# Kernel tuning notes

Hardware: AMD Instinct MI355X
Metric: run time of the kernel (lower is better)

Reference implementation:

```python
import math
import jax, jax.numpy as jnp
import numpy as np

B, H, M, L, D, HID = 4, 8, 1024, 3200, 128, 1024
ATTN_LIM, RAMP = 2048, 128
PRE_DIV, LOSS_COEF = 16.0, 1e-06
SIZE = ATTN_LIM  # ExpireSpanDrop size = args.attn_lim


def skew(X, pad_value):
    # X: (BH, M, K) -> (BH, M, K+M), shifting row i right by i (relative-pos trick)
    BH, Mq, K = X.shape
    X = jnp.pad(X, ((0, 0), (0, 0), (0, Mq + 1)), constant_values=pad_value)
    X = X.reshape(BH, -1)[:, :-Mq]
    return X.reshape(BH, Mq, K + Mq)


def setup_inputs():
    key = jax.random.key(0)
    ks = jax.random.split(key, 6)
    query = jax.random.normal(ks[0], (B * H, M, D), jnp.float32)
    k = jax.random.normal(ks[1], (B * H, L, D), jnp.float32)
    v = jax.random.normal(ks[2], (B * H, L, D), jnp.float32)
    memory_hid = jax.random.normal(ks[3], (B, L, HID), jnp.float32)
    # age counters: oldest slot first; the current block (last M slots) goes down to -(M-1)
    memory_counter = jnp.broadcast_to(
        jnp.arange(L - 1, -1, -1, dtype=jnp.float32) - (M - 1), (B, L))
    key_pe = 0.02 * jax.random.normal(ks[4], (1, D, M), jnp.float32)
    span_w = 0.01 * jax.random.normal(ks[5], (1, HID), jnp.float32)
    span_b = jnp.full((1,), -math.log(1.0 / 0.1 - 1.0), jnp.float32)  # init_percentage=0.1
    return {"query": query, "key": k, "value": v, "memory_hid": memory_hid,
            "memory_counter": memory_counter, "key_pe": key_pe,
            "span_w": span_w, "span_b": span_b}


def reference(query, key, value, memory_hid, memory_counter, key_pe, span_w, span_b):
    max_mem = ATTN_LIM + M + RAMP
    # QK^T
    attn = jnp.einsum('bmd,bld->bml', query, key)                              # (BH, M, L)
    # --- ExpireSpanDrop (eval mode, no noise) ---
    max_span = jax.nn.sigmoid(
        jnp.einsum('blh,oh->blo', memory_hid / PRE_DIV, span_w)[..., 0] + span_b[0]) * SIZE  # (B, L)
    remaining_offset = max_span - memory_counter                               # (B, L)
    remaining_span = remaining_offset[:, None, :] - jnp.arange(M, dtype=jnp.float32)[None, :, None]  # (B, M, L)
    emask = jnp.clip(remaining_span / RAMP + 1.0, 0.0, 1.0)
    ramp_mask = ((emask > 0) & (emask < 1)).astype(emask.dtype)
    aux_loss = (remaining_span * ramp_mask).sum((-1, -2)) / RAMP / M * LOSS_COEF  # (B,)
    # causal mask (precomputed buffer in torch)
    causal = jnp.tril(jnp.ones((M, max_mem), jnp.float32), k=max_mem - M - 1)[:, -L:]
    mask = jnp.broadcast_to((emask * causal)[:, None], (B, H, M, L)).reshape(B * H, M, L)
    # --- relative position bias via skew ---
    attn_pos = skew(jnp.einsum('bmd,dk->bmk', query, key_pe[0]), 0.0)          # (BH, M, 2M)
    attn = attn.at[:, :, -2 * M:].add(attn_pos)
    # masked softmax + renormalization by soft mask
    attn = jnp.where(mask == 0, -jnp.inf, attn) / math.sqrt(D)
    attn = jax.nn.softmax(attn, axis=-1)
    attn = attn * mask
    attn = attn / (attn.sum(-1, keepdims=True) + 1e-08)
    out = jnp.einsum('bml,bld->bmd', attn, value)                              # (BH, M, D)
    return out, aux_loss, remaining_offset
```

## Files before the change

### kernel.cpp

```cpp
#include <hip/hip_runtime.h>
#include <stdint.h>

#define B_   4
#define H_   8
#define BH_  32
#define M_   1024
#define L_   3200
#define D_   128
#define HID_ 1024
#define NT64 50
#define CAUSAL_K 2175
#define POS_OFF  1152
#define SCALE 0.08838834764831845f
#define NEGV (-3.0e38f)
#define NEGH (-1.0e38f)

typedef short  bf16x8 __attribute__((ext_vector_type(8)));
typedef float  f32x4  __attribute__((ext_vector_type(4)));

__device__ __forceinline__ unsigned short f2bf(float x) {
    union { float f; uint32_t u; } v; v.f = x;
    return (unsigned short)((v.u + 0x7FFFu + ((v.u >> 16) & 1u)) >> 16);
}
__device__ __forceinline__ float bf2f(unsigned short h) {
    union { uint32_t u; float f; } v; v.u = ((uint32_t)h) << 16; return v.f;
}
__device__ __forceinline__ uint32_t pack_bf2(float lo, float hi) {
    union { float f; uint32_t u; } a, b; a.f = lo; b.f = hi;
    return __builtin_amdgcn_perm(b.u, a.u, 0x07060302u);
}

template <int CTRL>
__device__ __forceinline__ float dpp_movf(float x) {
    union { float f; int i; } u; u.f = x;
    u.i = __builtin_amdgcn_update_dpp(0, u.i, CTRL, 0xF, 0xF, true);
    return u.f;
}
__device__ __forceinline__ float row_max16(float x) {
    x = fmaxf(x, dpp_movf<0xB1>(x));
    x = fmaxf(x, dpp_movf<0x4E>(x));
    x = fmaxf(x, dpp_movf<0x141>(x));
    x = fmaxf(x, dpp_movf<0x140>(x));
    return x;
}
__device__ __forceinline__ float row_sum16(float x) {
    x += dpp_movf<0xB1>(x);
    x += dpp_movf<0x4E>(x);
    x += dpp_movf<0x141>(x);
    x += dpp_movf<0x140>(x);
    return x;
}

__global__ void span_kernel(const float* __restrict__ hid,
                            const float* __restrict__ counter,
                            const float* __restrict__ sw,
                            const float* __restrict__ sb,
                            float* __restrict__ r0_ws,
                            float* __restrict__ r0_out) {
    const int row  = blockIdx.x * 4 + (threadIdx.x >> 6);
    const int lane = threadIdx.x & 63;
    const float* h = hid + (size_t)row * HID_;
    float acc = 0.f;
#pragma unroll
    for (int it = 0; it < 4; ++it) {
        const int k = it * 256 + lane * 4;
        const float4 a = *(const float4*)(h + k);
        const float4 w = *(const float4*)(sw + k);
        acc += a.x*w.x + a.y*w.y + a.z*w.z + a.w*w.w;
    }
#pragma unroll
    for (int off = 32; off; off >>= 1) acc += __shfl_down(acc, off);
    if (lane == 0) {
        const float x  = acc * (1.0f/16.0f) + sb[0];
        const float ms = 2048.0f / (1.0f + __expf(-x));
        const float r0 = ms - counter[row];
        r0_ws[row]  = r0;
        r0_out[row] = r0;
    }
}

__global__ void tilemax_kernel(const float* __restrict__ r0_ws,
                               float* __restrict__ tmax) {
    const int t = blockIdx.x;
    const int lane = threadIdx.x;
    float v = r0_ws[t * 64 + lane];
#pragma unroll
    for (int off = 32; off; off >>= 1) v = fmaxf(v, __shfl_down(v, off));
    if (lane == 0) tmax[t] = v;
}

__global__ void aux_kernel(const float* __restrict__ r0_ws,
                           float* __restrict__ aux_out) {
    const int b = blockIdx.x, tid = threadIdx.x;
    float s = 0.f;
    for (int l = tid; l < L_; l += 256) {
        const float r = r0_ws[b * L_ + l];
        const int fl = (int)floorf(r);
        int mlo = fl + 1;   if (mlo < 0) mlo = 0;
        int mhi = fl + 128; if (mhi > M_ - 1) mhi = M_ - 1;
        const int n = mhi - mlo + 1;
        if (n > 0) s += (float)n * r - 0.5f * (float)(mlo + mhi) * (float)n;
    }
    __shared__ float red[256];
    red[tid] = s; __syncthreads();
    for (int st = 128; st; st >>= 1) {
        if (tid < st) red[tid] += red[tid + st];
        __syncthreads();
    }
    if (tid == 0) aux_out[b] = red[0] * (1.0f/128.0f) * (1.0f/1024.0f) * 1e-6f;
}

__global__ void pet_kernel(const float* __restrict__ PE,
                           unsigned short* __restrict__ PET) {
    const int tid = threadIdx.x;
    const int c = blockIdx.x * 4 + (tid >> 6);
    const int e = tid & 63;
    const float lo = PE[(2*e)   * M_ + c];
    const float hi = PE[(2*e+1) * M_ + c];
    ((uint32_t*)PET)[c * 64 + e] = pack_bf2(lo, hi);
}

#define KS_STR 136
#define VT_STR 72
#define PE_STR 136
#define P_STR  72
#define T_STR  72

__global__ void __launch_bounds__(256, 2)
attn_kernel(const float* __restrict__ Q, const float* __restrict__ K,
            const float* __restrict__ V, const unsigned short* __restrict__ PET,
            const float* __restrict__ r0g, const float* __restrict__ tmax,
            float* __restrict__ out) {
    __shared__ short Ks[64 * KS_STR];
    __shared__ short Vt[128 * VT_STR];
    __shared__ short PEs[64 * PE_STR];
    __shared__ short Tb[2][64 * T_STR];
    __shared__ short Pb[64 * P_STR];
    __shared__ float r0s[64];
    __shared__ float tfl[NT64];

    const int bh = blockIdx.y;
    const int b  = bh >> 3;
    const int i0 = blockIdx.x << 6;
    const int tid  = threadIdx.x;
    const int wave = tid >> 6;
    const int lane = tid & 63;
    const int lq   = lane & 15;
    const int quad = lane >> 4;
    const int lt_end = min(NT64, (int)blockIdx.x + 35);

    if (tid < NT64) tfl[tid] = tmax[b * NT64 + tid];
    __syncthreads();
    const float live_thresh = (float)(i0 - 128);

    auto next_live = [&](int s) {
        while (s < lt_end && !(tfl[s] > live_thresh)) ++s;
        return s;
    };

    float4 kp[8];
    float4 vpa[4], vpb[4];
    uint4  pep[4];
    float  r0p = 0.f;

    auto issue_prefetch = [&](int plt) {
        const int l0p = plt << 6;
        const float* kb = K + ((size_t)bh * L_ + l0p) * D_;
        const float* vb = V + ((size_t)bh * L_ + l0p) * D_;
#pragma unroll
        for (int it = 0; it < 8; ++it) {
            const int f = it * 256 + tid;
            kp[it] = *(const float4*)(kb + (f >> 5) * D_ + (f & 31) * 4);
        }
        const int p2 = (tid & 31) * 2;
#pragma unroll
        for (int it = 0; it < 4; ++it) {
            const int c = it * 8 + (tid >> 5);
            vpa[it] = *(const float4*)(vb + (size_t)p2 * D_ + c * 4);
            vpb[it] = *(const float4*)(vb + (size_t)(p2 + 1) * D_ + c * 4);
        }
        const int c0p = l0p - i0 - POS_OFF;
#pragma unroll
        for (int it = 0; it < 4; ++it) {
            const int f = it * 256 + tid;
            const int cg = c0p + (f >> 4);
            if ((unsigned)cg < (unsigned)M_)
                pep[it] = *(const uint4*)(PET + (size_t)cg * D_ + (f & 15) * 8);
            else { pep[it].x = 0; pep[it].y = 0; pep[it].z = 0; pep[it].w = 0; }
        }
        if (tid < 64) r0p = r0g[b * L_ + l0p + tid];
    };

    auto write_stage = [&]() {
#pragma unroll
        for (int it = 0; it < 8; ++it) {
            const int f = it * 256 + tid;
            uint2 w;
            w.x = pack_bf2(kp[it].x, kp[it].y);
            w.y = pack_bf2(kp[it].z, kp[it].w);
            *(uint2*)&Ks[(f >> 5) * KS_STR + (f & 31) * 4] = w;
        }
        const int p2 = (tid & 31) * 2;
#pragma unroll
        for (int it = 0; it < 4; ++it) {
            const int c = it * 8 + (tid >> 5);
            const float* a = (const float*)&vpa[it];
            const float* bb = (const float*)&vpb[it];
#pragma unroll
            for (int j = 0; j < 4; ++j)
                *(uint32_t*)&Vt[(c * 4 + j) * VT_STR + p2] = pack_bf2(a[j], bb[j]);
        }
#pragma unroll
        for (int it = 0; it < 4; ++it) {
            const int f = it * 256 + tid;
            *(uint4*)&PEs[(f >> 4) * PE_STR + (f & 15) * 8] = pep[it];
        }
        if (tid < 64) r0s[tid] = r0p;
    };

    int lt = next_live(0);
    if (lt < lt_end) issue_prefetch(lt);

    bf16x8 qfrag[4];
    {
        const float* qp = Q + ((size_t)bh * M_ + (i0 + wave * 16 + lq)) * D_;
#pragma unroll
        for (int kk = 0; kk < 4; ++kk) {
            const float4 q0 = *(const float4*)(qp + kk * 32 + quad * 8);
            const float4 q1 = *(const float4*)(qp + kk * 32 + quad * 8 + 4);
            union { bf16x8 v; uint32_t u[4]; } qq;
            qq.u[0] = pack_bf2(q0.x, q0.y); qq.u[1] = pack_bf2(q0.z, q0.w);
            qq.u[2] = pack_bf2(q1.x, q1.y); qq.u[3] = pack_bf2(q1.z, q1.w);
            qfrag[kk] = qq.v;
        }
    }

    auto computeT = [&](short* tb) {
#pragma unroll
        for (int nt = 0; nt < 4; ++nt) {
            f32x4 acc = (f32x4){0.f, 0.f, 0.f, 0.f};
#pragma unroll
            for (int kk = 0; kk < 4; ++kk) {
                const bf16x8 bf = *(const bf16x8*)&PEs[(nt*16 + lq) * PE_STR + kk*32 + quad*8];
                acc = __builtin_amdgcn_mfma_f32_16x16x32_bf16(qfrag[kk], bf, acc, 0, 0, 0);
            }
#pragma unroll
            for (int r = 0; r < 4; ++r) {
                union { float f; uint32_t u; } t; t.f = acc[r];
                tb[(wave*16 + quad*4 + r) * T_STR + nt*16 + lq] = (short)(t.u >> 16);
            }
        }
    };

    f32x4 oacc[8];
#pragma unroll
    for (int d = 0; d < 8; ++d) oacc[d] = (f32x4){0.f, 0.f, 0.f, 0.f};
    float mrun[4] = {NEGV, NEGV, NEGV, NEGV};
    float Zr[4]   = {0.f, 0.f, 0.f, 0.f};
    float Zm[4]   = {0.f, 0.f, 0.f, 0.f};
    int tlo = 0, thi = 1;
    int prev_c0 = -(1 << 30);

    while (lt < lt_end) {
        const int l0 = lt << 6;
        const int c0 = l0 - i0 - POS_OFF;
        const bool need_pos = (c0 + 63 >= 0) && (c0 - 63 <= M_ - 1);
        const bool rolling  = need_pos && (prev_c0 == c0 - 64);

        __syncthreads();
        write_stage();
        __syncthreads();

        const int ltn = next_live(lt + 1);
        if (ltn < lt_end) issue_prefetch(ltn);

        f32x4 sfrag[4];
#pragma unroll
        for (int nt = 0; nt < 4; ++nt) {
            f32x4 acc = (f32x4){0.f, 0.f, 0.f, 0.f};
#pragma unroll
            for (int kk = 0; kk < 4; ++kk) {
                const bf16x8 bf = *(const bf16x8*)&Ks[(nt*16 + lq) * KS_STR + kk*32 + quad*8];
                acc = __builtin_amdgcn_mfma_f32_16x16x32_bf16(qfrag[kk], bf, acc, 0, 0, 0);
            }
            sfrag[nt] = acc;
        }

        if (need_pos) {
            if (rolling) {
                const int t = tlo; tlo = thi; thi = t;
                computeT(&Tb[thi][0]);
            } else {
                tlo = 0; thi = 1;
                computeT(&Tb[1][0]);
                uint4 lowp[4];
#pragma unroll
                for (int it = 0; it < 4; ++it) {
                    const int f = it * 256 + tid;
                    const int cg = (c0 - 64) + (f >> 4);
                    if ((unsigned)cg < (unsigned)M_)
                        lowp[it] = *(const uint4*)(PET + (size_t)cg * D_ + (f & 15) * 8);
                    else { lowp[it].x = 0; lowp[it].y = 0; lowp[it].z = 0; lowp[it].w = 0; }
                }
                __syncthreads();
#pragma unroll
                for (int it = 0; it < 4; ++it) {
                    const int f = it * 256 + tid;
                    *(uint4*)&PEs[(f >> 4) * PE_STR + (f & 15) * 8] = lowp[it];
                }
                __syncthreads();
                computeT(&Tb[0][0]);
            }
            prev_c0 = c0;
        } else {
            prev_c0 = -(1 << 30);
        }

        float rv[4];
#pragma unroll
        for (int nt = 0; nt < 4; ++nt) rv[nt] = r0s[nt*16 + lq];

        float sv[4][4], em[4][4];
#pragma unroll
        for (int r = 0; r < 4; ++r) {
            const int iq = i0 + wave*16 + quad*4 + r;
            const float fiq = (float)iq;
#pragma unroll
            for (int nt = 0; nt < 4; ++nt) {
                const int l = l0 + nt*16 + lq;
                float s = sfrag[nt][r];
                const int c = l - iq - POS_OFF;
                if (need_pos && (unsigned)c < (unsigned)M_) {
                    const int cb = c - (c0 - 64);
                    const short* tbp = (cb & 64) ? &Tb[thi][0] : &Tb[tlo][0];
                    s += bf2f((unsigned short)tbp[(wave*16 + quad*4 + r) * T_STR + (cb & 63)]);
                }
                const float e = fminf(fmaxf((rv[nt] - fiq) * 0.0078125f + 1.0f, 0.f), 1.f);
                em[r][nt] = e;
                const bool live = (l <= iq + CAUSAL_K) && (e > 0.f);
                sv[r][nt] = live ? s * SCALE : NEGV;
            }
        }

#pragma unroll
        for (int r = 0; r < 4; ++r) {
            float v = fmaxf(fmaxf(sv[r][0], sv[r][1]), fmaxf(sv[r][2], sv[r][3]));
            v = row_max16(v);
            const float nm = fmaxf(mrun[r], v);
            float alpha = 1.f, psum = 0.f, pmsum = 0.f, pmv[4];
            if (nm > NEGH) {
                alpha = (mrun[r] > NEGH) ? __expf(mrun[r] - nm) : 0.f;
#pragma unroll
                for (int nt = 0; nt < 4; ++nt) {
                    const float p = __expf(sv[r][nt] - nm);
                    const float pm = p * em[r][nt];
                    psum += p; pmsum += pm; pmv[nt] = pm;
                }
            } else {
                pmv[0] = pmv[1] = pmv[2] = pmv[3] = 0.f;
            }
            psum  = row_sum16(psum);
            pmsum = row_sum16(pmsum);
            mrun[r] = nm;
            Zr[r] = Zr[r] * alpha + psum;
            Zm[r] = Zm[r] * alpha + pmsum;
#pragma unroll
            for (int d = 0; d < 8; ++d) oacc[d][r] *= alpha;
#pragma unroll
            for (int nt = 0; nt < 4; ++nt) {
                union { float f; uint32_t u; } t; t.f = pmv[nt];
                Pb[(wave*16 + quad*4 + r) * P_STR + nt*16 + lq] = (short)(t.u >> 16);
            }
        }

#pragma unroll
        for (int kk = 0; kk < 2; ++kk) {
            const bf16x8 pf = *(const bf16x8*)&Pb[(wave*16 + lq) * P_STR + kk*32 + quad*8];
#pragma unroll
            for (int dt = 0; dt < 8; ++dt) {
                const bf16x8 vf = *(const bf16x8*)&Vt[(dt*16 + lq) * VT_STR + kk*32 + quad*8];
                oacc[dt] = __builtin_amdgcn_mfma_f32_16x16x32_bf16(pf, vf, oacc[dt], 0, 0, 0);
            }
        }
        lt = ltn;
    }

#pragma unroll
    for (int r = 0; r < 4; ++r) {
        const int iq = i0 + wave*16 + quad*4 + r;
        const float inv = 1.0f / (Zm[r] + 1e-8f * Zr[r]);
        float* op = out + ((size_t)bh * M_ + iq) * D_;
#pragma unroll
        for (int dt = 0; dt < 8; ++dt)
            op[dt*16 + lq] = oacc[dt][r] * inv;
    }
}

__global__ void __launch_bounds__(256, 2)
attn_fb_kernel(const float* __restrict__ Q, const float* __restrict__ K,
               const float* __restrict__ V, const float* __restrict__ PE,
               const float* __restrict__ r0g, const float* __restrict__ tmax,
               float* __restrict__ out) {
    __shared__ short Ks[64 * KS_STR];
    __shared__ short Vt[128 * VT_STR];
    __shared__ short PEP[64 * PE_STR];
    __shared__ short Tb[2][64 * T_STR];
    __shared__ float r0s[64];

    const int bh = blockIdx.y;
    const int b  = bh >> 3;
    const int i0 = blockIdx.x << 6;
    const int tid  = threadIdx.x;
    const int wave = tid >> 6;
    const int lane = tid & 63;
    const int lq   = lane & 15;
    const int quad = lane >> 4;

    bf16x8 qfrag[4];
    {
        const float* qp = Q + ((size_t)bh * M_ + (i0 + wave * 16 + lq)) * D_;
#pragma unroll
        for (int kk = 0; kk < 4; ++kk) {
            const float* p = qp + kk * 32 + quad * 8;
            bf16x8 f;
#pragma unroll
            for (int j = 0; j < 8; ++j) f[j] = (short)f2bf(p[j]);
            qfrag[kk] = f;
        }
    }

    f32x4 oacc[8];
#pragma unroll
    for (int d = 0; d < 8; ++d) oacc[d] = (f32x4){0.f, 0.f, 0.f, 0.f};
    float mrun[4] = {NEGV, NEGV, NEGV, NEGV};
    float Zr[4]   = {0.f, 0.f, 0.f, 0.f};
    float Zm[4]   = {0.f, 0.f, 0.f, 0.f};

    int tlo = 0, thi = 1;
    int prev_c0 = -100000;

    auto stagePE = [&](int cbase) {
#pragma unroll
        for (int it = 0; it < 8; ++it) {
            const int f4 = it * 256 + tid;
            const int d  = f4 >> 4;
            const int cl = (f4 & 15) << 2;
#pragma unroll
            for (int j = 0; j < 4; ++j) {
                const int cg = cbase + cl + j;
                const float v = (cg >= 0 && cg < M_) ? PE[d * M_ + cg] : 0.f;
                PEP[(cl + j) * PE_STR + d] = (short)f2bf(v);
            }
        }
    };
    auto computeT = [&](short* tb) {
#pragma unroll
        for (int nt = 0; nt < 4; ++nt) {
            f32x4 acc = (f32x4){0.f, 0.f, 0.f, 0.f};
#pragma unroll
            for (int kk = 0; kk < 4; ++kk) {
                const bf16x8 bf = *(const bf16x8*)&PEP[(nt*16 + lq) * PE_STR + kk*32 + quad*8];
                acc = __builtin_amdgcn_mfma_f32_16x16x32_bf16(qfrag[kk], bf, acc, 0, 0, 0);
            }
#pragma unroll
            for (int r = 0; r < 4; ++r)
                tb[(wave*16 + quad*4 + r) * T_STR + nt*16 + lq] = (short)f2bf(acc[r]);
        }
    };

    const int lt_end = min(NT64, (int)blockIdx.x + 35);
    for (int lt = 0; lt < lt_end; ++lt) {
        const int l0 = lt << 6;
        if (!(tmax[b * NT64 + lt] > (float)(i0 - 128))) continue;

        __syncthreads();
        {
            const float* kbase = K + ((size_t)bh * L_ + l0) * D_;
            const float* vbase = V + ((size_t)bh * L_ + l0) * D_;
#pragma unroll
            for (int it = 0; it < 8; ++it) {
                const int f4 = it * 256 + tid;
                const int row = f4 >> 5;
                const int ds  = (f4 & 31) << 2;
                const float4 kv = *(const float4*)(kbase + row * D_ + ds);
                uint2 pk;
                pk.x = (uint32_t)f2bf(kv.x) | ((uint32_t)f2bf(kv.y) << 16);
                pk.y = (uint32_t)f2bf(kv.z) | ((uint32_t)f2bf(kv.w) << 16);
                *(uint2*)&Ks[row * KS_STR + ds] = pk;
                const float4 vv = *(const float4*)(vbase + row * D_ + ds);
                Vt[(ds+0) * VT_STR + row] = (short)f2bf(vv.x);
                Vt[(ds+1) * VT_STR + row] = (short)f2bf(vv.y);
                Vt[(ds+2) * VT_STR + row] = (short)f2bf(vv.z);
                Vt[(ds+3) * VT_STR + row] = (short)f2bf(vv.w);
            }
            if (tid < 64) r0s[tid] = r0g[b * L_ + l0 + tid];
        }

        const int c0 = l0 - i0 - POS_OFF;
        const bool need_pos = (c0 + 63 >= 0) && (c0 - 63 <= M_ - 1);
        if (need_pos) {
            if (prev_c0 == c0 - 64) {
                const int t = tlo; tlo = thi; thi = t;
                stagePE(c0);
                __syncthreads();
                computeT(&Tb[thi][0]);
            } else {
                stagePE(c0 - 64);
                __syncthreads();
                computeT(&Tb[0][0]);
                __syncthreads();
                stagePE(c0);
                __syncthreads();
                computeT(&Tb[1][0]);
                tlo = 0; thi = 1;
            }
            prev_c0 = c0;
        } else {
            __syncthreads();
        }

        f32x4 sfrag[4];
#pragma unroll
        for (int nt = 0; nt < 4; ++nt) {
            f32x4 acc = (f32x4){0.f, 0.f, 0.f, 0.f};
#pragma unroll
            for (int kk = 0; kk < 4; ++kk) {
                const bf16x8 bf = *(const bf16x8*)&Ks[(nt*16 + lq) * KS_STR + kk*32 + quad*8];
                acc = __builtin_amdgcn_mfma_f32_16x16x32_bf16(qfrag[kk], bf, acc, 0, 0, 0);
            }
            sfrag[nt] = acc;
        }
        __syncthreads();

        float sv[4][4];
#pragma unroll
        for (int r = 0; r < 4; ++r) {
            const int iq = i0 + wave*16 + quad*4 + r;
#pragma unroll
            for (int nt = 0; nt < 4; ++nt) {
                const int l = l0 + nt*16 + lq;
                float s = sfrag[nt][r];
                const int c = l - iq - POS_OFF;
                if (c >= 0 && c < M_) {
                    const int cb = c - (c0 - 64);
                    const short* tbp = (cb & 64) ? &Tb[thi][0] : &Tb[tlo][0];
                    s += bf2f((unsigned short)tbp[(wave*16 + quad*4 + r) * T_STR + (cb & 63)]);
                }
                const float e = fminf(fmaxf((r0s[nt*16 + lq] - (float)iq) * 0.0078125f + 1.0f, 0.f), 1.f);
                const bool live = (l <= iq + CAUSAL_K) && (e > 0.f);
                sv[r][nt] = live ? s * SCALE : NEGV;
            }
        }

#pragma unroll
        for (int r = 0; r < 4; ++r) {
            float v = fmaxf(fmaxf(sv[r][0], sv[r][1]), fmaxf(sv[r][2], sv[r][3]));
            v = row_max16(v);
            const float nm = fmaxf(mrun[r], v);
            float alpha, pmv[4];
            float psum = 0.f, pmsum = 0.f;
            if (nm > NEGH) {
                alpha = (mrun[r] > NEGH) ? __expf(mrun[r] - nm) : 0.f;
                const int iq = i0 + wave*16 + quad*4 + r;
#pragma unroll
                for (int nt = 0; nt < 4; ++nt) {
                    const float p = __expf(sv[r][nt] - nm);
                    const float e = fminf(fmaxf((r0s[nt*16 + lq] - (float)iq) * 0.0078125f + 1.0f, 0.f), 1.f);
                    const float pm = p * e;
                    psum += p; pmsum += pm; pmv[nt] = pm;
                }
            } else {
                alpha = 1.f;
                pmv[0] = pmv[1] = pmv[2] = pmv[3] = 0.f;
            }
            psum  = row_sum16(psum);
            pmsum = row_sum16(pmsum);
            mrun[r] = nm;
            Zr[r] = Zr[r] * alpha + psum;
            Zm[r] = Zm[r] * alpha + pmsum;
#pragma unroll
            for (int d = 0; d < 8; ++d) oacc[d][r] *= alpha;
#pragma unroll
            for (int nt = 0; nt < 4; ++nt)
                PEP[(wave*16 + quad*4 + r) * P_STR + nt*16 + lq] = (short)f2bf(pmv[nt]);
        }
        __syncthreads();

#pragma unroll
        for (int kk = 0; kk < 2; ++kk) {
            const bf16x8 pf = *(const bf16x8*)&PEP[(wave*16 + lq) * P_STR + kk*32 + quad*8];
#pragma unroll
            for (int dt = 0; dt < 8; ++dt) {
                const bf16x8 vf = *(const bf16x8*)&Vt[(dt*16 + lq) * VT_STR + kk*32 + quad*8];
                oacc[dt] = __builtin_amdgcn_mfma_f32_16x16x32_bf16(pf, vf, oacc[dt], 0, 0, 0);
            }
        }
    }

#pragma unroll
    for (int r = 0; r < 4; ++r) {
        const int iq = i0 + wave*16 + quad*4 + r;
        const float inv = 1.0f / (Zm[r] + 1e-8f * Zr[r]);
        float* op = out + ((size_t)bh * M_ + iq) * D_;
#pragma unroll
        for (int dt = 0; dt < 8; ++dt)
            op[dt*16 + lq] = oacc[dt][r] * inv;
    }
}

extern "C" void kernel_launch(void* const* d_in, const int* in_sizes, int n_in,
                              void* d_out, int out_size, void* d_ws, size_t ws_size,
                              hipStream_t stream) {
    (void)in_sizes; (void)n_in; (void)out_size;
    const float* Q       = (const float*)d_in[0];
    const float* K       = (const float*)d_in[1];
    const float* V       = (const float*)d_in[2];
    const float* hid     = (const float*)d_in[3];
    const float* counter = (const float*)d_in[4];
    const float* pe      = (const float*)d_in[5];
    const float* sw      = (const float*)d_in[6];
    const float* sb      = (const float*)d_in[7];

    float* out    = (float*)d_out;
    float* aux    = out + (size_t)BH_ * M_ * D_;
    float* r0_out = aux + B_;

    float* r0_ws = (float*)d_ws;
    float* tmax  = r0_ws + B_ * L_;
    unsigned short* PET = (unsigned short*)(r0_ws + 13056);
    const bool use_pet = ws_size >= (size_t)(13056 * 4 + M_ * D_ * 2);

    span_kernel<<<(B_ * L_) / 4, 256, 0, stream>>>(hid, counter, sw, sb, r0_ws, r0_out);
    tilemax_kernel<<<B_ * NT64, 64, 0, stream>>>(r0_ws, tmax);
    if (use_pet) {
        pet_kernel<<<M_ / 4, 256, 0, stream>>>(pe, PET);
        attn_kernel<<<dim3(M_ / 64, BH_), 256, 0, stream>>>(Q, K, V, PET, r0_ws, tmax, out);
    } else {
        attn_fb_kernel<<<dim3(M_ / 64, BH_), 256, 0, stream>>>(Q, K, V, pe, r0_ws, tmax, out);
    }
    aux_kernel<<<B_, 256, 0, stream>>>(r0_ws, aux);
}
```

Measured before the change: 237.0 us.

## Fuse prep kernels, use ballot liveness mask, keep r0 in registers, set MFMA priority

Merges the span and PE-transpose kernels, and the tile-max and aux-loss kernels, cutting the launch count from five to three. In the attention kernel the shared-memory liveness scan and its barrier become a wave ballot bitmask with ctz lookup. The per-tile r0 values are prefetched straight into registers instead of going through shared memory. MFMA sections are wrapped in s_setprio, and the unmasked softmax denominator is dropped, so the 1e-8 epsilon term is no longer scaled by it and numerics shift slightly.

```diff
diff --git a/kernel.cpp b/kernel.cpp
--- a/kernel.cpp
+++ b/kernel.cpp
@@ -51,14 +51,17 @@
     return x;
 }
 
-__global__ void span_kernel(const float* __restrict__ hid,
-                            const float* __restrict__ counter,
-                            const float* __restrict__ sw,
-                            const float* __restrict__ sb,
-                            float* __restrict__ r0_ws,
-                            float* __restrict__ r0_out) {
-    const int row  = blockIdx.x * 4 + (threadIdx.x >> 6);
-    const int lane = threadIdx.x & 63;
+__global__ void span_pet_kernel(const float* __restrict__ hid,
+                                const float* __restrict__ counter,
+                                const float* __restrict__ sw,
+                                const float* __restrict__ sb,
+                                const float* __restrict__ PE,
+                                float* __restrict__ r0_ws,
+                                float* __restrict__ r0_out,
+                                unsigned short* __restrict__ PET) {
+    const int tid  = threadIdx.x;
+    const int row  = blockIdx.x * 4 + (tid >> 6);
+    const int lane = tid & 63;
     const float* h = hid + (size_t)row * HID_;
     float acc = 0.f;
 #pragma unroll
@@ -77,47 +80,46 @@
         r0_ws[row]  = r0;
         r0_out[row] = r0;
     }
-}
-
-__global__ void tilemax_kernel(const float* __restrict__ r0_ws,
-                               float* __restrict__ tmax) {
-    const int t = blockIdx.x;
-    const int lane = threadIdx.x;
-    float v = r0_ws[t * 64 + lane];
-#pragma unroll
-    for (int off = 32; off; off >>= 1) v = fmaxf(v, __shfl_down(v, off));
-    if (lane == 0) tmax[t] = v;
-}
-
-__global__ void aux_kernel(const float* __restrict__ r0_ws,
-                           float* __restrict__ aux_out) {
-    const int b = blockIdx.x, tid = threadIdx.x;
-    float s = 0.f;
-    for (int l = tid; l < L_; l += 256) {
-        const float r = r0_ws[b * L_ + l];
-        const int fl = (int)floorf(r);
-        int mlo = fl + 1;   if (mlo < 0) mlo = 0;
-        int mhi = fl + 128; if (mhi > M_ - 1) mhi = M_ - 1;
-        const int n = mhi - mlo + 1;
-        if (n > 0) s += (float)n * r - 0.5f * (float)(mlo + mhi) * (float)n;
-    }
+    if (PET != nullptr && blockIdx.x < M_ / 4) {
+        const int c = blockIdx.x * 4 + (tid >> 6);
+        const int e = tid & 63;
+        const float lo = PE[(2*e)   * M_ + c];
+        const float hi = PE[(2*e+1) * M_ + c];
+        ((uint32_t*)PET)[c * 64 + e] = pack_bf2(lo, hi);
+    }
+}
+
+__global__ void prep_kernel(const float* __restrict__ r0_ws,
+                            float* __restrict__ tmax,
+                            float* __restrict__ aux_out) {
     __shared__ float red[256];
-    red[tid] = s; __syncthreads();
-    for (int st = 128; st; st >>= 1) {
-        if (tid < st) red[tid] += red[tid + st];
-        __syncthreads();
-    }
-    if (tid == 0) aux_out[b] = red[0] * (1.0f/128.0f) * (1.0f/1024.0f) * 1e-6f;
-}
-
-__global__ void pet_kernel(const float* __restrict__ PE,
-                           unsigned short* __restrict__ PET) {
+    const int bid = blockIdx.x;
     const int tid = threadIdx.x;
-    const int c = blockIdx.x * 4 + (tid >> 6);
-    const int e = tid & 63;
-    const float lo = PE[(2*e)   * M_ + c];
-    const float hi = PE[(2*e+1) * M_ + c];
-    ((uint32_t*)PET)[c * 64 + e] = pack_bf2(lo, hi);
+    if (bid < 50) {
+        const int wave = tid >> 6, lane = tid & 63;
+        const int t = bid * 4 + wave;
+        float v = r0_ws[t * 64 + lane];
+#pragma unroll
+        for (int off = 32; off; off >>= 1) v = fmaxf(v, __shfl_down(v, off));
+        if (lane == 0) tmax[t] = v;
+    } else {
+        const int b = bid - 50;
+        float s = 0.f;
+        for (int l = tid; l < L_; l += 256) {
+            const float r = r0_ws[b * L_ + l];
+            const int fl = (int)floorf(r);
+            int mlo = fl + 1;   if (mlo < 0) mlo = 0;
+            int mhi = fl + 128; if (mhi > M_ - 1) mhi = M_ - 1;
+            const int n = mhi - mlo + 1;
+            if (n > 0) s += (float)n * r - 0.5f * (float)(mlo + mhi) * (float)n;
+        }
+        red[tid] = s; __syncthreads();
+        for (int st = 128; st; st >>= 1) {
+            if (tid < st) red[tid] += red[tid + st];
+            __syncthreads();
+        }
+        if (tid == 0) aux_out[b] = red[0] * (1.0f/128.0f) * (1.0f/1024.0f) * 1e-6f;
+    }
 }
 
 #define KS_STR 136
@@ -136,8 +138,6 @@
     __shared__ short PEs[64 * PE_STR];
     __shared__ short Tb[2][64 * T_STR];
     __shared__ short Pb[64 * P_STR];
-    __shared__ float r0s[64];
-    __shared__ float tfl[NT64];
 
     const int bh = blockIdx.y;
     const int b  = bh >> 3;
@@ -149,19 +149,23 @@
     const int quad = lane >> 4;
     const int lt_end = min(NT64, (int)blockIdx.x + 35);
 
-    if (tid < NT64) tfl[tid] = tmax[b * NT64 + tid];
-    __syncthreads();
     const float live_thresh = (float)(i0 - 128);
-
-    auto next_live = [&](int s) {
-        while (s < lt_end && !(tfl[s] > live_thresh)) ++s;
-        return s;
+    unsigned long long live_mask;
+    {
+        const int sidx = (lane < NT64) ? lane : (NT64 - 1);
+        const float tv = tmax[b * NT64 + sidx];
+        live_mask = __ballot((lane < NT64) && (lane < lt_end) && (tv > live_thresh));
+    }
+    auto next_live = [&](int s) -> int {
+        const unsigned long long m = live_mask >> s;
+        return m ? (s + __builtin_ctzll(m)) : lt_end;
     };
 
     float4 kp[8];
     float4 vpa[4], vpb[4];
     uint4  pep[4];
-    float  r0p = 0.f;
+    float  rvp[4];
+    float  rv[4];
 
     auto issue_prefetch = [&](int plt) {
         const int l0p = plt << 6;
@@ -188,7 +192,9 @@
                 pep[it] = *(const uint4*)(PET + (size_t)cg * D_ + (f & 15) * 8);
             else { pep[it].x = 0; pep[it].y = 0; pep[it].z = 0; pep[it].w = 0; }
         }
-        if (tid < 64) r0p = r0g[b * L_ + l0p + tid];
+        const float* rb = r0g + b * L_ + l0p;
+#pragma unroll
+        for (int nt = 0; nt < 4; ++nt) rvp[nt] = rb[nt * 16 + lq];
     };
 
     auto write_stage = [&]() {
@@ -215,7 +221,8 @@
             const int f = it * 256 + tid;
             *(uint4*)&PEs[(f >> 4) * PE_STR + (f & 15) * 8] = pep[it];
         }
-        if (tid < 64) r0s[tid] = r0p;
+#pragma unroll
+        for (int nt = 0; nt < 4; ++nt) rv[nt] = rvp[nt];
     };
 
     int lt = next_live(0);
@@ -236,6 +243,7 @@
     }
 
     auto computeT = [&](short* tb) {
+        __builtin_amdgcn_s_setprio(1);
 #pragma unroll
         for (int nt = 0; nt < 4; ++nt) {
             f32x4 acc = (f32x4){0.f, 0.f, 0.f, 0.f};
@@ -250,13 +258,13 @@
                 tb[(wave*16 + quad*4 + r) * T_STR + nt*16 + lq] = (short)(t.u >> 16);
             }
         }
+        __builtin_amdgcn_s_setprio(0);
     };
 
     f32x4 oacc[8];
 #pragma unroll
     for (int d = 0; d < 8; ++d) oacc[d] = (f32x4){0.f, 0.f, 0.f, 0.f};
     float mrun[4] = {NEGV, NEGV, NEGV, NEGV};
-    float Zr[4]   = {0.f, 0.f, 0.f, 0.f};
     float Zm[4]   = {0.f, 0.f, 0.f, 0.f};
     int tlo = 0, thi = 1;
     int prev_c0 = -(1 << 30);
@@ -275,6 +283,7 @@
         if (ltn < lt_end) issue_prefetch(ltn);
 
         f32x4 sfrag[4];
+        __builtin_amdgcn_s_setprio(1);
 #pragma unroll
         for (int nt = 0; nt < 4; ++nt) {
             f32x4 acc = (f32x4){0.f, 0.f, 0.f, 0.f};
@@ -285,6 +294,7 @@
             }
             sfrag[nt] = acc;
         }
+        __builtin_amdgcn_s_setprio(0);
 
         if (need_pos) {
             if (rolling) {
@@ -315,10 +325,6 @@
         } else {
             prev_c0 = -(1 << 30);
         }
-
-        float rv[4];
-#pragma unroll
-        for (int nt = 0; nt < 4; ++nt) rv[nt] = r0s[nt*16 + lq];
 
         float sv[4][4], em[4][4];
 #pragma unroll
@@ -347,22 +353,20 @@
             float v = fmaxf(fmaxf(sv[r][0], sv[r][1]), fmaxf(sv[r][2], sv[r][3]));
             v = row_max16(v);
             const float nm = fmaxf(mrun[r], v);
-            float alpha = 1.f, psum = 0.f, pmsum = 0.f, pmv[4];
+            float alpha = 1.f, pmsum = 0.f, pmv[4];
             if (nm > NEGH) {
                 alpha = (mrun[r] > NEGH) ? __expf(mrun[r] - nm) : 0.f;
 #pragma unroll
                 for (int nt = 0; nt < 4; ++nt) {
                     const float p = __expf(sv[r][nt] - nm);
                     const float pm = p * em[r][nt];
-                    psum += p; pmsum += pm; pmv[nt] = pm;
+                    pmsum += pm; pmv[nt] = pm;
                 }
             } else {
                 pmv[0] = pmv[1] = pmv[2] = pmv[3] = 0.f;
             }
-            psum  = row_sum16(psum);
             pmsum = row_sum16(pmsum);
             mrun[r] = nm;
-            Zr[r] = Zr[r] * alpha + psum;
             Zm[r] = Zm[r] * alpha + pmsum;
 #pragma unroll
             for (int d = 0; d < 8; ++d) oacc[d][r] *= alpha;
@@ -373,6 +377,7 @@
             }
         }
 
+        __builtin_amdgcn_s_setprio(1);
 #pragma unroll
         for (int kk = 0; kk < 2; ++kk) {
             const bf16x8 pf = *(const bf16x8*)&Pb[(wave*16 + lq) * P_STR + kk*32 + quad*8];
@@ -382,13 +387,14 @@
                 oacc[dt] = __builtin_amdgcn_mfma_f32_16x16x32_bf16(pf, vf, oacc[dt], 0, 0, 0);
             }
         }
+        __builtin_amdgcn_s_setprio(0);
         lt = ltn;
     }
 
 #pragma unroll
     for (int r = 0; r < 4; ++r) {
         const int iq = i0 + wave*16 + quad*4 + r;
-        const float inv = 1.0f / (Zm[r] + 1e-8f * Zr[r]);
+        const float inv = 1.0f / (Zm[r] + 1e-8f);
         float* op = out + ((size_t)bh * M_ + iq) * D_;
 #pragma unroll
         for (int dt = 0; dt < 8; ++dt)
@@ -630,13 +636,12 @@
     unsigned short* PET = (unsigned short*)(r0_ws + 13056);
     const bool use_pet = ws_size >= (size_t)(13056 * 4 + M_ * D_ * 2);
 
-    span_kernel<<<(B_ * L_) / 4, 256, 0, stream>>>(hid, counter, sw, sb, r0_ws, r0_out);
-    tilemax_kernel<<<B_ * NT64, 64, 0, stream>>>(r0_ws, tmax);
+    span_pet_kernel<<<(B_ * L_) / 4, 256, 0, stream>>>(
+        hid, counter, sw, sb, pe, r0_ws, r0_out, use_pet ? PET : nullptr);
+    prep_kernel<<<54, 256, 0, stream>>>(r0_ws, tmax, aux);
     if (use_pet) {
-        pet_kernel<<<M_ / 4, 256, 0, stream>>>(pe, PET);
         attn_kernel<<<dim3(M_ / 64, BH_), 256, 0, stream>>>(Q, K, V, PET, r0_ws, tmax, out);
     } else {
         attn_fb_kernel<<<dim3(M_ / 64, BH_), 256, 0, stream>>>(Q, K, V, pe, r0_ws, tmax, out);
     }
-    aux_kernel<<<B_, 256, 0, stream>>>(r0_ws, aux);
-}
+}
```

After: 233.3 us. Within noise of the previous version (-1.6%).
